# Performance work log

Hardware: AMD Instinct MI355X
Metric: run time of the kernel (lower is better)

## Reference

```python
import jax, jax.numpy as jnp
import numpy as np

B, N, NT, MAXN, M2, TF = 1, 4096, 2, 100, 16, 4
NA = N // NT          # atoms per type
J = NT * MAXN         # total neighbor slots per atom
GDIM = 100
D = M2 * GDIM         # fitting-net input dim
FH = 240


def _mlp_emb(x, w0, b0, w1, b1, w2, b2):
    h = jnp.tanh(x @ w0 + b0)
    h = jnp.tanh(h @ w1 + b1)
    return jnp.tanh(h @ w2 + b2)


def _mlp_fit(x, w0, b0, w1, b1, w2, b2):
    h = jnp.tanh(x @ w0 + b0)
    h = jnp.tanh(h @ w1 + b1)
    return h @ w2 + b2


def setup_inputs() -> dict:
    key = jax.random.key(0)
    ks = jax.random.split(key, 16)

    def w(k, shape):
        return (jax.random.normal(k, shape, jnp.float32) / np.float32(np.sqrt(shape[-2])))

    return {
        "Ri": jax.random.normal(ks[0], (B, N, J, 4), jnp.float32),
        "dfeat": jax.random.normal(ks[1], (B, N, J, 4, 3), jnp.float32),
        "ImageDR": jax.random.normal(ks[2], (B, N, J, 3), jnp.float32),
        "type_vector": jax.random.uniform(ks[3], (NT, TF), jnp.float32),
        "ew0": w(ks[4], (1 + TF, 25)), "eb0": jnp.zeros((25,), jnp.float32),
        "ew1": w(ks[5], (25, 50)), "eb1": jnp.zeros((50,), jnp.float32),
        "ew2": w(ks[6], (50, GDIM)), "eb2": jnp.zeros((GDIM,), jnp.float32),
        "fw0": w(ks[7], (NT, D, FH)), "fb0": jnp.zeros((NT, FH), jnp.float32),
        "fw1": w(ks[8], (NT, FH, FH)), "fb1": jnp.zeros((NT, FH), jnp.float32),
        "fw2": w(ks[9], (NT, FH, 1)),
        "fb2": jnp.full((NT, 1), -3.0, jnp.float32),  # energy_shift folded into bias
        "list_neigh": jax.random.randint(ks[10], (B, N, J), 0, N + 1, dtype=jnp.int32),
    }


def reference(Ri, dfeat, ImageDR, type_vector, ew0, eb0, ew1, eb1, ew2, eb2,
              fw0, fb0, fw1, fb1, fw2, fb2, list_neigh):
    # type embedding feature, repeated per neighbor slot: [J, TF]
    temb = jnp.repeat(type_vector, MAXN, axis=0)

    def energy(Ri_):
        parts = []
        for t in range(NT):  # small fixed loop over atom types
            a = Ri_[:, t * NA:(t + 1) * NA]                      # [B,NA,J,4]
            x = jnp.concatenate(
                [a[..., :1], jnp.broadcast_to(temb, (B, NA, J, TF))], axis=-1)
            G = _mlp_emb(x, ew0, eb0, ew1, eb1, ew2, eb2)        # [B,NA,J,GDIM]
            xa = jnp.einsum('bnjc,bnjg->bncg', a, G) / (MAXN * NT)
            dr = jnp.einsum('bncg,bncm->bngm', xa, xa[..., :M2]).reshape(B, NA, D)
            parts.append(_mlp_fit(dr, fw0[t], fb0[t], fw1[t], fb1[t], fw2[t], fb2[t]))
        return jnp.concatenate(parts, axis=1)                    # [B,N,1]

    Ei = energy(Ri)
    Etot = jnp.sum(Ei, axis=1)                                   # [B,1]

    # dE/dRi (autograd.grad with ones mask == grad of sum(Ei))
    dE = jax.grad(lambda r: energy(r).sum())(Ri)                 # [B,N,J,4]
    dE_dx = jnp.einsum('bnjc,bnjcd->bnjd', dE, dfeat)            # [B,N,J,3]
    F = -jnp.sum(dE_dx, axis=2)                                  # -dE @ Ri_d (all slots)

    mask = (list_neigh > 0).astype(Ri.dtype)[..., None]
    contrib = dE_dx * mask                                       # only real neighbors
    idx = jnp.clip(list_neigh - 1, 0, N - 1)

    def scat(Fb, ib, cb):
        return Fb.at[ib.reshape(-1)].add(cb.reshape(-1, 3))
    F = jax.vmap(scat)(F, idx, contrib)

    dr0, dr1, dr2 = ImageDR[..., 0], ImageDR[..., 1], ImageDR[..., 2]
    c0, c1, c2 = contrib[..., 0], contrib[..., 1], contrib[..., 2]
    s = lambda v: jnp.sum(v, axis=(1, 2))
    V00, V11, V22 = s(dr0 * c0), s(dr1 * c1), s(dr2 * c2)
    V01, V02, V12 = s(dr0 * c1), s(dr0 * c2), s(dr1 * c2)
    Virial = jnp.stack([V00, V01, V02, V01, V11, V12, V02, V12, V22], axis=-1)

    return (Etot, jnp.squeeze(Ei, 2), F, Virial)
```

## Files before the change

### kernel.cpp

```cpp
#include <hip/hip_runtime.h>

#define NATOMS 4096
#define NTYPES 2
#define NA 2048
#define MAXNB 100
#define JN 200
#define TFD 4
#define E0 25
#define E1 50
#define GD 100
#define M2D 16
#define DD 1600
#define FHD 240
#define INV200 (1.0f/200.0f)

#define OUT_EI 1
#define OUT_F 4097
#define OUT_V 16385

#define WS_Q 0L
#define WS_FW1T 0L
#define WS_DRB 6553600L
#define WS_XA 9830400L
#define WS_P 11468800L
#define WS_FH0 13107200L
#define WS_FH1 14090240L
#define WS_DH0GB 15073280L
#define WS_FH0B 15597568L
#define WS_FW0TB 16121856L
#define WS_FW0B 16531456L
#define WS_FW1TB 16941056L

#define NK 1024
#define S_MIN (-8.0f)
#define S_H 0.015625f
#define S_INVH 64.0f
#define HCH 104
__device__ float4 g_tab4[NTYPES * NK * GD];
__device__ float2 g_th1[NTYPES * NK * E1];
__device__ _Float16 h_tab[NTYPES * NK * HCH * 4];

typedef __attribute__((ext_vector_type(8))) short bf16x8;
typedef __attribute__((ext_vector_type(4))) float f32x4;
typedef __attribute__((ext_vector_type(2))) _Float16 h16x2;

#if defined(__has_builtin)
#if __has_builtin(__builtin_amdgcn_fdot2)
#define HAVE_FDOT2 1
#endif
#endif
#ifdef HAVE_FDOT2
#define FDOT2(a, b, c) __builtin_amdgcn_fdot2((a), (b), (c), false)
#else
__device__ __forceinline__ float fdot2_sw(h16x2 a, h16x2 b, float c) {
    return fmaf((float)a[0], (float)b[0], fmaf((float)a[1], (float)b[1], c));
}
#define FDOT2(a, b, c) fdot2_sw((a), (b), (c))
#endif

__device__ __forceinline__ h16x2 as_h2(unsigned u) {
    union { unsigned u; h16x2 h; } v; v.u = u; return v.h;
}

__device__ __forceinline__ unsigned h2u(h16x2 h) {
    union { h16x2 h; unsigned u; } v; v.h = h; return v.u;
}

__device__ __forceinline__ float ftanh(float x) {
    float ax = fabsf(x);
    float e = __expf(-2.0f * ax);
    float t = (1.0f - e) / (1.0f + e);
    return copysignf(t, x);
}

__device__ __forceinline__ unsigned short f2b(float f) {
    union { float f; unsigned u; } v; v.f = f;
    unsigned r = (v.u + 0x7FFF + ((v.u >> 16) & 1)) >> 16;
    return (unsigned short)r;
}

__device__ __forceinline__ float4 ntload4(const float4* p) {
    f32x4 v = __builtin_nontemporal_load((const f32x4*)p);
    float4 r; r.x = v.x; r.y = v.y; r.z = v.z; r.w = v.w;
    return r;
}

__global__ void k_setup(const float* __restrict__ fw0, const float* __restrict__ fw1,
                        unsigned short* __restrict__ fw0Tb, unsigned short* __restrict__ fw0b,
                        float* __restrict__ fw1T, unsigned short* __restrict__ fw1Tb) {
    int idx = blockIdx.x * 256 + threadIdx.x;
    if (idx < NTYPES * FHD * DD) {
        int t = idx / (FHD * DD);
        int r = idx % (FHD * DD);
        int o = r / DD, d = r % DD;
        fw0Tb[(long)t * 256 * DD + (long)o * DD + d] =
            f2b(fw0[(long)t * DD * FHD + (long)d * FHD + o]);
    }
    if (idx < NTYPES * DD * 256) {
        int t = idx / (DD * 256);
        int r = idx % (DD * 256);
        int d = r / 256, kk = r % 256;
        float v = (kk < FHD) ? fw0[(long)t * DD * FHD + (long)d * FHD + kk] : 0.f;
        fw0b[idx] = f2b(v);
    }
    if (idx < NTYPES * FHD * FHD) {
        int t = idx / (FHD * FHD);
        int r = idx % (FHD * FHD);
        int o = r / FHD, i = r % FHD;
        fw1T[idx] = fw1[(long)t * FHD * FHD + (long)i * FHD + o];
    }
    if (idx < NTYPES * FHD * 256) {
        int t = idx / (FHD * 256);
        int r = idx % (FHD * 256);
        int o = r / 256, kk = r % 256;
        float v = (kk < FHD) ? fw1[(long)t * FHD * FHD + (long)kk * FHD + o] : 0.f;
        fw1Tb[(long)t * 256 * 256 + (long)o * 256 + kk] = f2b(v);
    }
}

__global__ __launch_bounds__(256) void k_table_h(
    const float* __restrict__ ew0, const float* __restrict__ eb0,
    const float* __restrict__ ew1, const float* __restrict__ eb1,
    const float* __restrict__ tv)
{
    int idx = blockIdx.x * 256 + threadIdx.x;
    if (idx >= NTYPES * NK) return;
    int t = idx / NK, i = idx % NK;
    float s = S_MIN + (float)i * S_H;

    float h0[E0], t0[E0];
#pragma unroll
    for (int k = 0; k < E0; ++k) {
        float c = eb0[k];
#pragma unroll
        for (int f = 0; f < TFD; ++f) c = fmaf(tv[t * TFD + f], ew0[(1 + f) * E0 + k], c);
        float h = ftanh(fmaf(s, ew0[k], c));
        h0[k] = h;
        t0[k] = (1.f - h * h) * ew0[k];
    }
#pragma unroll 2
    for (int l = 0; l < E1; ++l) {
        float acc = eb1[l], dacc = 0.f;
#pragma unroll
        for (int k = 0; k < E0; ++k) {
            float w = ew1[k * E1 + l];
            acc = fmaf(h0[k], w, acc);
            dacc = fmaf(t0[k], w, dacc);
        }
        float h = ftanh(acc);
        g_th1[(long)idx * E1 + l] = make_float2(h, (1.f - h * h) * dacc);
    }
}

__global__ __launch_bounds__(256) void k_table_g(
    const float* __restrict__ ew2, const float* __restrict__ eb2)
{
    long idx = (long)blockIdx.x * 256 + threadIdx.x;
    if (idx >= (long)NTYPES * NK * GD) return;
    int g = idx % GD;
    long ti = idx / GD;
    int i = ti % NK;

    const float2* hv = g_th1 + ti * E1;
    float acc = eb2[g], dacc = 0.f;
#pragma unroll 5
    for (int l = 0; l < E1; ++l) {
        float2 x = hv[l];
        float w = ew2[l * GD + g];
        acc = fmaf(x.x, w, acc);
        dacc = fmaf(x.y, w, dacc);
    }
    float G = ftanh(acc);
    float dv = (1.f - G * G) * dacc;

    float2* f2 = (float2*)g_tab4;
    long e = ti * GD + g;
    f2[2 * e] = make_float2(G, dv);
    if (i > 0) f2[2 * (e - GD) + 1] = make_float2(G, dv);
}

__global__ __launch_bounds__(256) void k_table_h16() {
    long idx = (long)blockIdx.x * 256 + threadIdx.x;
    if (idx >= (long)NTYPES * NK * HCH) return;
    int g = idx % HCH;
    long ti = idx / HCH;
    _Float16* dst = h_tab + idx * 4;
    if (g >= GD) {
        dst[0] = (_Float16)0.f; dst[1] = (_Float16)0.f;
        dst[2] = (_Float16)0.f; dst[3] = (_Float16)0.f;
        return;
    }
    float4 r = g_tab4[ti * GD + g];
    dst[0] = (_Float16)r.x;
    dst[1] = (_Float16)(r.z - r.x);
    dst[2] = (_Float16)r.y;
    dst[3] = (_Float16)r.w;
}

__device__ __forceinline__ int hermite6(float s,
    float& c01, float& c10, float& c11,
    float& d00, float& d10, float& d11)
{
    float x = (s - S_MIN) * S_INVH;
    x = fminf(fmaxf(x, 0.f), (float)(NK - 1) - 1e-3f);
    int i = (int)x;
    float u = x - (float)i;
    float um = 1.f - u;
    c01 = u * u * (3.f - 2.f * u);
    c10 = S_H * u * um * um;
    c11 = S_H * u * u * (u - 1.f);
    d00 = (6.f * u * u - 6.f * u) * S_INVH;
    d10 = fmaf(3.f * u, u, fmaf(-4.f, u, 1.f));
    d11 = fmaf(3.f * u, u, -2.f * u);
    return i;
}

__global__ __launch_bounds__(256) void k1_emb(
    const float* __restrict__ Ri,
    unsigned short* __restrict__ drb, float* __restrict__ xa_ws)
{
    __shared__ float4 a4s[JN];
    __shared__ uint2 cpak[JN];
    __shared__ int rowoff[JN];
    __shared__ float xar[4 * 400];
    __shared__ float xas[400];

    int tid = threadIdx.x;
    int lane = tid & 63;
    int w = tid >> 6;
    int n = blockIdx.x;

    if (tid < JN) {
        float4 a = ((const float4*)Ri)[(long)n * JN + tid];
        a4s[tid] = a;
        float c01, c10, c11, d00, d10, d11;
        int ik = hermite6(a.x, c01, c10, c11, d00, d10, d11);
        rowoff[tid] = ((tid / MAXNB) * NK + ik) * (HCH / 2);
        h16x2 cP; cP[0] = (_Float16)1.f;  cP[1] = (_Float16)c01;
        h16x2 cQ; cQ[0] = (_Float16)c10;  cQ[1] = (_Float16)c11;
        cpak[tid] = make_uint2(h2u(cP), h2u(cQ));
    }
    __syncthreads();

    float xe0 = 0.f, xe1 = 0.f, xe2 = 0.f, xe3 = 0.f;
    float xo0 = 0.f, xo1 = 0.f, xo2 = 0.f, xo3 = 0.f;

#pragma unroll 4
    for (int ii = 0; ii < 50; ++ii) {
        int j = w * 50 + ii;
        uint2 cc = cpak[j];
        const uint4* row4 = (const uint4*)h_tab + rowoff[j];
        if (lane < 50) {
            uint4 v = row4[lane];
            float4 a = a4s[j];
            float Ge = FDOT2(as_h2(v.y), as_h2(cc.y), FDOT2(as_h2(v.x), as_h2(cc.x), 0.f));
            float Go = FDOT2(as_h2(v.w), as_h2(cc.y), FDOT2(as_h2(v.z), as_h2(cc.x), 0.f));
            xe0 = fmaf(a.x, Ge, xe0); xe1 = fmaf(a.y, Ge, xe1);
            xe2 = fmaf(a.z, Ge, xe2); xe3 = fmaf(a.w, Ge, xe3);
            xo0 = fmaf(a.x, Go, xo0); xo1 = fmaf(a.y, Go, xo1);
            xo2 = fmaf(a.z, Go, xo2); xo3 = fmaf(a.w, Go, xo3);
        }
    }

    float* xw = xar + w * 400;
    if (lane < 50) {
        *(float2*)&xw[0 * GD + 2 * lane] = make_float2(xe0, xo0);
        *(float2*)&xw[1 * GD + 2 * lane] = make_float2(xe1, xo1);
        *(float2*)&xw[2 * GD + 2 * lane] = make_float2(xe2, xo2);
        *(float2*)&xw[3 * GD + 2 * lane] = make_float2(xe3, xo3);
    }
    __syncthreads();

    for (int i = tid; i < 400; i += 256) {
        float v = (xar[i] + xar[400 + i] + xar[800 + i] + xar[1200 + i]) * INV200;
        xas[i] = v;
        xa_ws[(long)n * 400 + i] = v;
    }
    __syncthreads();

    for (int i = tid; i < DD; i += 256) {
        int gg = i / M2D, m = i % M2D;
        float v = 0.f;
#pragma unroll
        for (int c = 0; c < 4; ++c) v = fmaf(xas[c * GD + gg], xas[c * GD + m], v);
        drb[(long)n * DD + i] = f2b(v);
    }
}

__global__ __launch_bounds__(256) void mgemm(
    const unsigned short* __restrict__ Ab, const unsigned short* __restrict__ BTb,
    const float* __restrict__ biasb, float* __restrict__ Cb, unsigned short* __restrict__ Cbf,
    int M, int N, int K, int Npad,
    long sA, long sBT, long sBias, long sC, long sCbf, int do_tanh)
{
    int t = blockIdx.z;
    const unsigned short* A = Ab + (long)t * sA;
    const unsigned short* BT = BTb + (long)t * sBT;
    const float* bias = biasb ? biasb + (long)t * sBias : nullptr;
    float* C = Cb + (long)t * sC;
    unsigned short* Cb16 = Cbf ? Cbf + (long)t * sCbf : nullptr;

    __shared__ __align__(16) unsigned short As[64 * 72];
    __shared__ __align__(16) unsigned short Bs[64 * 72];

    int tid = threadIdx.x;
    int m0 = blockIdx.x * 64;
    int n0 = blockIdx.y * 64;

    int lane = tid & 63;
    int w = tid >> 6;
    int wm = (w & 1) * 32;
    int wn = (w >> 1) * 32;
    int fm = lane & 15;
    int q = lane >> 4;

    f32x4 acc[2][2] = {};

    int sr = tid >> 2;
    int sc = tid & 3;

    const unsigned short* Ar = A + (long)(m0 + sr) * K + sc * 8;
    const unsigned short* Br = BT + (long)(n0 + sr) * K + sc * 8;
    unsigned short* Asw = As + sr * 72 + sc * 8;
    unsigned short* Bsw = Bs + sr * 72 + sc * 8;

    for (int k0 = 0; k0 < K; k0 += 64) {
        uint4 av0 = *(const uint4*)(Ar + k0);
        uint4 av1 = *(const uint4*)(Ar + k0 + 32);
        uint4 bv0 = *(const uint4*)(Br + k0);
        uint4 bv1 = *(const uint4*)(Br + k0 + 32);
        __syncthreads();
        *(uint4*)(Asw) = av0;
        *(uint4*)(Asw + 32) = av1;
        *(uint4*)(Bsw) = bv0;
        *(uint4*)(Bsw + 32) = bv1;
        __syncthreads();
#pragma unroll
        for (int kk = 0; kk < 64; kk += 32) {
            bf16x8 af0 = *(const bf16x8*)(As + (wm + fm) * 72 + kk + q * 8);
            bf16x8 af1 = *(const bf16x8*)(As + (wm + 16 + fm) * 72 + kk + q * 8);
            bf16x8 bg0 = *(const bf16x8*)(Bs + (wn + fm) * 72 + kk + q * 8);
            bf16x8 bg1 = *(const bf16x8*)(Bs + (wn + 16 + fm) * 72 + kk + q * 8);
            acc[0][0] = __builtin_amdgcn_mfma_f32_16x16x32_bf16(af0, bg0, acc[0][0], 0, 0, 0);
            acc[0][1] = __builtin_amdgcn_mfma_f32_16x16x32_bf16(af0, bg1, acc[0][1], 0, 0, 0);
            acc[1][0] = __builtin_amdgcn_mfma_f32_16x16x32_bf16(af1, bg0, acc[1][0], 0, 0, 0);
            acc[1][1] = __builtin_amdgcn_mfma_f32_16x16x32_bf16(af1, bg1, acc[1][1], 0, 0, 0);
        }
    }

#pragma unroll
    for (int i = 0; i < 2; ++i) {
#pragma unroll
        for (int j = 0; j < 2; ++j) {
            int col = n0 + wn + j * 16 + fm;
            int rb = m0 + wm + i * 16 + q * 4;
            bool ok = col < N;
            float bv = (bias && ok) ? bias[col] : 0.f;
#pragma unroll
            for (int r = 0; r < 4; ++r) {
                float v = acc[i][j][r] + bv;
                if (do_tanh) v = ftanh(v);
                if (ok) C[(long)(rb + r) * N + col] = v;
                if (Cb16) Cb16[(long)(rb + r) * Npad + col] = ok ? f2b(v) : (unsigned short)0;
            }
        }
    }
}

__global__ __launch_bounds__(256) void k3a(
    const float* __restrict__ fh0, const float* __restrict__ fh1,
    const float* __restrict__ fw1T, const float* __restrict__ fw2, const float* __restrict__ fb2,
    float* __restrict__ out, unsigned short* __restrict__ dh0gb)
{
    int n = blockIdx.x;
    int t = n / NA;
    int tid = threadIdx.x;
    __shared__ float u1s[FHD];
    __shared__ float red[256];

    float p = 0.f;
    if (tid < FHD) {
        float h1v = fh1[(long)n * FHD + tid];
        float w2v = fw2[t * FHD + tid];
        p = h1v * w2v;
        u1s[tid] = w2v * (1.f - h1v * h1v);
    }
    red[tid] = p;
    __syncthreads();
    for (int off = 128; off > 0; off >>= 1) {
        if (tid < off) red[tid] += red[tid + off];
        __syncthreads();
    }
    if (tid == 0) {
        float e = red[0] + fb2[t];
        out[OUT_EI + n] = e;
        atomicAdd(out, e);
    }
    float val = 0.f;
    if (tid < FHD) {
        const float* wT = fw1T + (long)t * FHD * FHD;
        float acc = 0.f;
        for (int o = 0; o < FHD; ++o) acc = fmaf(u1s[o], wT[o * FHD + tid], acc);
        float h0v = fh0[(long)n * FHD + tid];
        val = acc * (1.f - h0v * h0v);
    }
    dh0gb[(long)n * 256 + tid] = (tid < FHD) ? f2b(val) : (unsigned short)0;
}

__global__ __launch_bounds__(256) void k3b(
    const float* __restrict__ Q, const float* __restrict__ xa, float* __restrict__ P4)
{
    int n = blockIdx.x;
    int tid = threadIdx.x;
    __shared__ float qs[DD];
    __shared__ float xs[400];
    for (int i = tid; i < DD; i += 256) qs[i] = Q[(long)n * DD + i];
    for (int i = tid; i < 400; i += 256) xs[i] = xa[(long)n * 400 + i];
    __syncthreads();
    for (int i = tid; i < 400; i += 256) {
        int c = i / GD, g = i % GD;
        float acc = 0.f;
        for (int m = 0; m < M2D; ++m) acc = fmaf(qs[g * M2D + m], xs[c * GD + m], acc);
        if (g < M2D) {
            for (int g2 = 0; g2 < GD; ++g2) acc = fmaf(qs[g2 * M2D + g], xs[c * GD + g2], acc);
        }
        P4[((long)n * GD + g) * 4 + c] = acc * INV200;
    }
}

__device__ __forceinline__ void k4_tail(
    int n, int j, float4 a,
    float M10, float M11, float M12, float M13,
    float M20, float M21, float M22, float M23,
    const float* __restrict__ dfeat, const float* __restrict__ ImageDR,
    const int* __restrict__ list_neigh, float* __restrict__ out, int ql,
    float& f0, float& f1, float& f2v,
    float& v00, float& v01, float& v02, float& v11, float& v12, float& v22)
{
    float ds = a.x * M20 + a.y * M21 + a.z * M22 + a.w * M23;
    float dEda0 = M10 + ds, dEda1 = M11, dEda2 = M12, dEda3 = M13;

    long item = (long)n * JN + j;
    if (ql < 3) {
        const float* dfp = dfeat + item * 12 + ql;
        float w0 = __builtin_nontemporal_load(dfp);
        float w1 = __builtin_nontemporal_load(dfp + 3);
        float w2 = __builtin_nontemporal_load(dfp + 6);
        float w3 = __builtin_nontemporal_load(dfp + 9);
        float dEdx = dEda0 * w0 + dEda1 * w1 + dEda2 * w2 + dEda3 * w3;

        if (ql == 0) f0 += dEdx;
        else if (ql == 1) f1 += dEdx;
        else f2v += dEdx;

        int ln = __builtin_nontemporal_load(list_neigh + item);
        if (ln > 0) {
            int ii2 = ln - 1;
            if (ii2 > NATOMS - 1) ii2 = NATOMS - 1;
            atomicAdd(&out[OUT_F + ii2 * 3 + ql], dEdx);
            float im0 = __builtin_nontemporal_load(ImageDR + item * 3);
            float im1 = __builtin_nontemporal_load(ImageDR + item * 3 + 1);
            float im2 = __builtin_nontemporal_load(ImageDR + item * 3 + 2);
            if (ql == 0) {
                v00 += im0 * dEdx;
            } else if (ql == 1) {
                v01 += im0 * dEdx; v11 += im1 * dEdx;
            } else {
                v02 += im0 * dEdx; v12 += im1 * dEdx; v22 += im2 * dEdx;
            }
        }
    }
}

__global__ __launch_bounds__(256, 4) void k4(
    const float* __restrict__ Ri, const float* __restrict__ dfeat,
    const float* __restrict__ ImageDR, const int* __restrict__ list_neigh,
    const float4* __restrict__ P4ws, float* __restrict__ out)
{
    __shared__ float4 a4s[JN];
    __shared__ float4 P4s[HCH];
    __shared__ float fred[4][3];
    __shared__ float vred[4][6];
    __shared__ float vacc[6];

    int tid = threadIdx.x;
    int lane = tid & 63;
    int w = tid >> 6;
    int n = blockIdx.x;

    if (tid < JN) a4s[tid] = ntload4(&((const float4*)Ri)[(long)n * JN + tid]);
    if (tid < HCH)
        P4s[tid] = (tid < GD) ? ntload4(&P4ws[(long)n * GD + tid])
                              : make_float4(0.f, 0.f, 0.f, 0.f);
    __syncthreads();

    int ql = lane & 3;
    int qid = w * 16 + (lane >> 2);

    float f0 = 0.f, f1 = 0.f, f2v = 0.f;
    float v00 = 0.f, v01 = 0.f, v02 = 0.f, v11 = 0.f, v12 = 0.f, v22 = 0.f;

    for (int pass = 0; pass < 4; ++pass) {
        int j;
        if (pass < 3) {
            j = pass * 64 + qid;
        } else {
            if (qid & 7) break;
            j = 192 + (qid >> 3);
        }

        float4 a = a4s[j];
        float c01, c10, c11, d00, d10, d11;
        int ik = hermite6(a.x, c01, c10, c11, d00, d10, d11);
        const uint4* row4 = (const uint4*)h_tab + (long)((j / MAXNB) * NK + ik) * (HCH / 2);

        h16x2 cP; cP[0] = (_Float16)1.f;   cP[1] = (_Float16)c01;
        h16x2 cQ; cQ[0] = (_Float16)c10;   cQ[1] = (_Float16)c11;
        h16x2 cR; cR[0] = (_Float16)0.f;   cR[1] = (_Float16)(-d00);
        h16x2 cS; cS[0] = (_Float16)d10;   cS[1] = (_Float16)d11;

        float M10 = 0.f, M11 = 0.f, M12 = 0.f, M13 = 0.f;
        float M20 = 0.f, M21 = 0.f, M22 = 0.f, M23 = 0.f;

        uint4 r[13];
#pragma unroll
        for (int i2 = 0; i2 < 13; ++i2) r[i2] = row4[4 * i2 + ql];
        __builtin_amdgcn_sched_barrier(0);

#pragma unroll
        for (int i2 = 0; i2 < 13; ++i2) {
            int ca = 8 * i2 + 2 * ql;
            float4 pa = P4s[ca];
            float4 pb = P4s[ca + 1];
            float G1 = FDOT2(as_h2(r[i2].y), cQ, FDOT2(as_h2(r[i2].x), cP, 0.f));
            float D1 = FDOT2(as_h2(r[i2].y), cS, FDOT2(as_h2(r[i2].x), cR, 0.f));
            M10 = fmaf(pa.x, G1, M10); M11 = fmaf(pa.y, G1, M11);
            M12 = fmaf(pa.z, G1, M12); M13 = fmaf(pa.w, G1, M13);
            M20 = fmaf(pa.x, D1, M20); M21 = fmaf(pa.y, D1, M21);
            M22 = fmaf(pa.z, D1, M22); M23 = fmaf(pa.w, D1, M23);
            float G2 = FDOT2(as_h2(r[i2].w), cQ, FDOT2(as_h2(r[i2].z), cP, 0.f));
            float D2 = FDOT2(as_h2(r[i2].w), cS, FDOT2(as_h2(r[i2].z), cR, 0.f));
            M10 = fmaf(pb.x, G2, M10); M11 = fmaf(pb.y, G2, M11);
            M12 = fmaf(pb.z, G2, M12); M13 = fmaf(pb.w, G2, M13);
            M20 = fmaf(pb.x, D2, M20); M21 = fmaf(pb.y, D2, M21);
            M22 = fmaf(pb.z, D2, M22); M23 = fmaf(pb.w, D2, M23);
        }
        __builtin_amdgcn_sched_barrier(0);

#pragma unroll
        for (int mask = 1; mask <= 2; mask <<= 1) {
            M10 += __shfl_xor(M10, mask); M11 += __shfl_xor(M11, mask);
            M12 += __shfl_xor(M12, mask); M13 += __shfl_xor(M13, mask);
            M20 += __shfl_xor(M20, mask); M21 += __shfl_xor(M21, mask);
            M22 += __shfl_xor(M22, mask); M23 += __shfl_xor(M23, mask);
        }

        k4_tail(n, j, a, M10, M11, M12, M13, M20, M21, M22, M23,
                dfeat, ImageDR, list_neigh, out, ql, f0, f1, f2v,
                v00, v01, v02, v11, v12, v22);
    }

#pragma unroll
    for (int mask = 32; mask > 0; mask >>= 1) {
        f0 += __shfl_xor(f0, mask);
        f1 += __shfl_xor(f1, mask);
        f2v += __shfl_xor(f2v, mask);
        v00 += __shfl_xor(v00, mask);
        v01 += __shfl_xor(v01, mask);
        v02 += __shfl_xor(v02, mask);
        v11 += __shfl_xor(v11, mask);
        v12 += __shfl_xor(v12, mask);
        v22 += __shfl_xor(v22, mask);
    }
    if (lane == 0) {
        fred[w][0] = f0; fred[w][1] = f1; fred[w][2] = f2v;
        vred[w][0] = v00; vred[w][1] = v01; vred[w][2] = v02;
        vred[w][3] = v11; vred[w][4] = v12; vred[w][5] = v22;
    }
    __syncthreads();
    if (tid < 3) {
        float s = fred[0][tid] + fred[1][tid] + fred[2][tid] + fred[3][tid];
        atomicAdd(&out[OUT_F + n * 3 + tid], -s);
    }
    if (tid < 6) {
        vacc[tid] = vred[0][tid] + vred[1][tid] + vred[2][tid] + vred[3][tid];
    }
    __syncthreads();
    if (tid < 9) {
        const int vmap[9] = {0, 1, 2, 1, 3, 4, 2, 4, 5};
        atomicAdd(&out[OUT_V + tid], vacc[vmap[tid]]);
    }
}

extern "C" void kernel_launch(void* const* d_in, const int* in_sizes, int n_in,
                              void* d_out, int out_size, void* d_ws, size_t ws_size,
                              hipStream_t stream) {
    const float* Ri = (const float*)d_in[0];
    const float* dfeat = (const float*)d_in[1];
    const float* ImageDR = (const float*)d_in[2];
    const float* tv = (const float*)d_in[3];
    const float* ew0 = (const float*)d_in[4];
    const float* eb0 = (const float*)d_in[5];
    const float* ew1 = (const float*)d_in[6];
    const float* eb1 = (const float*)d_in[7];
    const float* ew2 = (const float*)d_in[8];
    const float* eb2 = (const float*)d_in[9];
    const float* fw0 = (const float*)d_in[10];
    const float* fb0 = (const float*)d_in[11];
    const float* fw1 = (const float*)d_in[12];
    const float* fb1 = (const float*)d_in[13];
    const float* fw2 = (const float*)d_in[14];
    const float* fb2 = (const float*)d_in[15];
    const int* list_neigh = (const int*)d_in[16];

    float* out = (float*)d_out;
    float* ws = (float*)d_ws;
    float* Q = ws + WS_Q;
    float* fw1T = ws + WS_FW1T;
    unsigned short* drb = (unsigned short*)(ws + WS_DRB);
    float* xa = ws + WS_XA;
    float* P = ws + WS_P;
    float* fh0 = ws + WS_FH0;
    float* fh1 = ws + WS_FH1;
    unsigned short* dh0gb = (unsigned short*)(ws + WS_DH0GB);
    unsigned short* fh0b = (unsigned short*)(ws + WS_FH0B);
    unsigned short* fw0Tb = (unsigned short*)(ws + WS_FW0TB);
    unsigned short* fw0b = (unsigned short*)(ws + WS_FW0B);
    unsigned short* fw1Tb = (unsigned short*)(ws + WS_FW1TB);

    hipMemsetAsync(d_out, 0, (size_t)out_size * sizeof(float), stream);

    k_setup<<<(NTYPES * DD * 256 + 255) / 256, 256, 0, stream>>>(
        fw0, fw1, fw0Tb, fw0b, fw1T, fw1Tb);
    k_table_h<<<(NTYPES * NK + 255) / 256, 256, 0, stream>>>(ew0, eb0, ew1, eb1, tv);
    k_table_g<<<(NTYPES * NK * GD + 255) / 256, 256, 0, stream>>>(ew2, eb2);
    k_table_h16<<<(NTYPES * NK * HCH + 255) / 256, 256, 0, stream>>>();

    k1_emb<<<NATOMS, 256, 0, stream>>>(Ri, drb, xa);

    mgemm<<<dim3(32, 4, 2), 256, 0, stream>>>(
        drb, fw0Tb, fb0, fh0, fh0b,
        2048, 240, 1600, 256,
        2048L * 1600, 256L * 1600, 240L, 2048L * 240, 2048L * 256, 1);
    mgemm<<<dim3(32, 4, 2), 256, 0, stream>>>(
        fh0b, fw1Tb, fb1, fh1, nullptr,
        2048, 240, 256, 0,
        2048L * 256, 256L * 256, 240L, 2048L * 240, 0L, 1);

    k3a<<<NATOMS, 256, 0, stream>>>(fh0, fh1, fw1T, fw2, fb2, out, dh0gb);

    mgemm<<<dim3(32, 25, 2), 256, 0, stream>>>(
        dh0gb, fw0b, nullptr, Q, nullptr,
        2048, 1600, 256, 0,
        2048L * 256, 1600L * 256, 0L, 2048L * 1600, 0L, 0);

    k3b<<<NATOMS, 256, 0, stream>>>(Q, xa, P);

    k4<<<NATOMS, 256, 0, stream>>>(Ri, dfeat, ImageDR, list_neigh,
        (const float4*)P, out);
}
```

Before: 437.3 us.

## Move fitting-net layer-1 backprop matvec into bf16 MFMA GEMM with tanh-derivative epilogue

The per-atom scalar matvec in k3a (u1 times fw1 transposed, then times 1-h0^2) is replaced by a batched bf16 MFMA GEMM. k3a now only writes u1 as padded bf16, and a new mgemm mode multiplies by (1-x^2) in the epilogue while writing the bf16 dh0 directly. k_setup builds a padded bf16 copy of fw1 instead of the fp32 transpose. k4 launch bounds are also raised to 6 blocks per SM, which may raise register pressure, and rounding u1 and fw1 to bf16 lowers precision.

```diff
diff --git a/kernel.cpp b/kernel.cpp
--- a/kernel.cpp
+++ b/kernel.cpp
@@ -19,8 +19,9 @@
 #define OUT_V 16385
 
 #define WS_Q 0L
-#define WS_FW1T 0L
+#define WS_FW1NB 0L
 #define WS_DRB 6553600L
+#define WS_U1B 6553600L
 #define WS_XA 9830400L
 #define WS_P 11468800L
 #define WS_FH0 13107200L
@@ -87,7 +88,7 @@
 
 __global__ void k_setup(const float* __restrict__ fw0, const float* __restrict__ fw1,
                         unsigned short* __restrict__ fw0Tb, unsigned short* __restrict__ fw0b,
-                        float* __restrict__ fw1T, unsigned short* __restrict__ fw1Tb) {
+                        unsigned short* __restrict__ fw1Tb, unsigned short* __restrict__ fw1Nb) {
     int idx = blockIdx.x * 256 + threadIdx.x;
     if (idx < NTYPES * FHD * DD) {
         int t = idx / (FHD * DD);
@@ -103,18 +104,19 @@
         float v = (kk < FHD) ? fw0[(long)t * DD * FHD + (long)d * FHD + kk] : 0.f;
         fw0b[idx] = f2b(v);
     }
-    if (idx < NTYPES * FHD * FHD) {
-        int t = idx / (FHD * FHD);
-        int r = idx % (FHD * FHD);
-        int o = r / FHD, i = r % FHD;
-        fw1T[idx] = fw1[(long)t * FHD * FHD + (long)i * FHD + o];
-    }
     if (idx < NTYPES * FHD * 256) {
         int t = idx / (FHD * 256);
         int r = idx % (FHD * 256);
         int o = r / 256, kk = r % 256;
         float v = (kk < FHD) ? fw1[(long)t * FHD * FHD + (long)kk * FHD + o] : 0.f;
         fw1Tb[(long)t * 256 * 256 + (long)o * 256 + kk] = f2b(v);
+    }
+    if (idx < NTYPES * 256 * 256) {
+        int t = idx / (256 * 256);
+        int r = idx % (256 * 256);
+        int i = r / 256, kk = r % 256;
+        float v = (i < FHD && kk < FHD) ? fw1[(long)t * FHD * FHD + (long)i * FHD + kk] : 0.f;
+        fw1Nb[(long)t * 256 * 256 + (long)i * 256 + kk] = f2b(v);
     }
 }
 
@@ -290,15 +292,17 @@
 __global__ __launch_bounds__(256) void mgemm(
     const unsigned short* __restrict__ Ab, const unsigned short* __restrict__ BTb,
     const float* __restrict__ biasb, float* __restrict__ Cb, unsigned short* __restrict__ Cbf,
+    const float* __restrict__ Xb,
     int M, int N, int K, int Npad,
-    long sA, long sBT, long sBias, long sC, long sCbf, int do_tanh)
+    long sA, long sBT, long sBias, long sC, long sCbf, long sX, int mode)
 {
     int t = blockIdx.z;
     const unsigned short* A = Ab + (long)t * sA;
     const unsigned short* BT = BTb + (long)t * sBT;
     const float* bias = biasb ? biasb + (long)t * sBias : nullptr;
-    float* C = Cb + (long)t * sC;
+    float* C = Cb ? Cb + (long)t * sC : nullptr;
     unsigned short* Cb16 = Cbf ? Cbf + (long)t * sCbf : nullptr;
+    const float* X = Xb ? Xb + (long)t * sX : nullptr;
 
     __shared__ __align__(16) unsigned short As[64 * 72];
     __shared__ __align__(16) unsigned short Bs[64 * 72];
@@ -359,8 +363,13 @@
 #pragma unroll
             for (int r = 0; r < 4; ++r) {
                 float v = acc[i][j][r] + bv;
-                if (do_tanh) v = ftanh(v);
-                if (ok) C[(long)(rb + r) * N + col] = v;
+                if (mode == 1) {
+                    v = ftanh(v);
+                } else if (mode == 2 && ok) {
+                    float x = X[(long)(rb + r) * N + col];
+                    v *= (1.f - x * x);
+                }
+                if (ok && C) C[(long)(rb + r) * N + col] = v;
                 if (Cb16) Cb16[(long)(rb + r) * Npad + col] = ok ? f2b(v) : (unsigned short)0;
             }
         }
@@ -368,23 +377,23 @@
 }
 
 __global__ __launch_bounds__(256) void k3a(
-    const float* __restrict__ fh0, const float* __restrict__ fh1,
-    const float* __restrict__ fw1T, const float* __restrict__ fw2, const float* __restrict__ fb2,
-    float* __restrict__ out, unsigned short* __restrict__ dh0gb)
+    const float* __restrict__ fh1, const float* __restrict__ fw2,
+    const float* __restrict__ fb2,
+    float* __restrict__ out, unsigned short* __restrict__ u1b)
 {
     int n = blockIdx.x;
     int t = n / NA;
     int tid = threadIdx.x;
-    __shared__ float u1s[FHD];
     __shared__ float red[256];
 
-    float p = 0.f;
+    float p = 0.f, u1 = 0.f;
     if (tid < FHD) {
         float h1v = fh1[(long)n * FHD + tid];
         float w2v = fw2[t * FHD + tid];
         p = h1v * w2v;
-        u1s[tid] = w2v * (1.f - h1v * h1v);
-    }
+        u1 = w2v * (1.f - h1v * h1v);
+    }
+    u1b[(long)n * 256 + tid] = (tid < FHD) ? f2b(u1) : (unsigned short)0;
     red[tid] = p;
     __syncthreads();
     for (int off = 128; off > 0; off >>= 1) {
@@ -396,15 +405,6 @@
         out[OUT_EI + n] = e;
         atomicAdd(out, e);
     }
-    float val = 0.f;
-    if (tid < FHD) {
-        const float* wT = fw1T + (long)t * FHD * FHD;
-        float acc = 0.f;
-        for (int o = 0; o < FHD; ++o) acc = fmaf(u1s[o], wT[o * FHD + tid], acc);
-        float h0v = fh0[(long)n * FHD + tid];
-        val = acc * (1.f - h0v * h0v);
-    }
-    dh0gb[(long)n * 256 + tid] = (tid < FHD) ? f2b(val) : (unsigned short)0;
 }
 
 __global__ __launch_bounds__(256) void k3b(
@@ -472,7 +472,7 @@
     }
 }
 
-__global__ __launch_bounds__(256, 4) void k4(
+__global__ __launch_bounds__(256, 6) void k4(
     const float* __restrict__ Ri, const float* __restrict__ dfeat,
     const float* __restrict__ ImageDR, const int* __restrict__ list_neigh,
     const float4* __restrict__ P4ws, float* __restrict__ out)
@@ -616,8 +616,9 @@
     float* out = (float*)d_out;
     float* ws = (float*)d_ws;
     float* Q = ws + WS_Q;
-    float* fw1T = ws + WS_FW1T;
+    unsigned short* fw1Nb = (unsigned short*)(ws + WS_FW1NB);
     unsigned short* drb = (unsigned short*)(ws + WS_DRB);
+    unsigned short* u1b = (unsigned short*)(ws + WS_U1B);
     float* xa = ws + WS_XA;
     float* P = ws + WS_P;
     float* fh0 = ws + WS_FH0;
@@ -631,7 +632,7 @@
     hipMemsetAsync(d_out, 0, (size_t)out_size * sizeof(float), stream);
 
     k_setup<<<(NTYPES * DD * 256 + 255) / 256, 256, 0, stream>>>(
-        fw0, fw1, fw0Tb, fw0b, fw1T, fw1Tb);
+        fw0, fw1, fw0Tb, fw0b, fw1Tb, fw1Nb);
     k_table_h<<<(NTYPES * NK + 255) / 256, 256, 0, stream>>>(ew0, eb0, ew1, eb1, tv);
     k_table_g<<<(NTYPES * NK * GD + 255) / 256, 256, 0, stream>>>(ew2, eb2);
     k_table_h16<<<(NTYPES * NK * HCH + 255) / 256, 256, 0, stream>>>();
@@ -639,20 +640,25 @@
     k1_emb<<<NATOMS, 256, 0, stream>>>(Ri, drb, xa);
 
     mgemm<<<dim3(32, 4, 2), 256, 0, stream>>>(
-        drb, fw0Tb, fb0, fh0, fh0b,
+        drb, fw0Tb, fb0, fh0, fh0b, nullptr,
         2048, 240, 1600, 256,
-        2048L * 1600, 256L * 1600, 240L, 2048L * 240, 2048L * 256, 1);
+        2048L * 1600, 256L * 1600, 240L, 2048L * 240, 2048L * 256, 0L, 1);
     mgemm<<<dim3(32, 4, 2), 256, 0, stream>>>(
-        fh0b, fw1Tb, fb1, fh1, nullptr,
+        fh0b, fw1Tb, fb1, fh1, nullptr, nullptr,
         2048, 240, 256, 0,
-        2048L * 256, 256L * 256, 240L, 2048L * 240, 0L, 1);
-
-    k3a<<<NATOMS, 256, 0, stream>>>(fh0, fh1, fw1T, fw2, fb2, out, dh0gb);
+        2048L * 256, 256L * 256, 240L, 2048L * 240, 0L, 0L, 1);
+
+    k3a<<<NATOMS, 256, 0, stream>>>(fh1, fw2, fb2, out, u1b);
+
+    mgemm<<<dim3(32, 4, 2), 256, 0, stream>>>(
+        u1b, fw1Nb, nullptr, nullptr, dh0gb, fh0,
+        2048, 240, 256, 256,
+        2048L * 256, 256L * 256, 0L, 0L, 2048L * 256, 2048L * 240, 2);
 
     mgemm<<<dim3(32, 25, 2), 256, 0, stream>>>(
-        dh0gb, fw0b, nullptr, Q, nullptr,
+        dh0gb, fw0b, nullptr, Q, nullptr, nullptr,
         2048, 1600, 256, 0,
-        2048L * 256, 1600L * 256, 0L, 2048L * 1600, 0L, 0);
+        2048L * 256, 1600L * 256, 0L, 2048L * 1600, 0L, 0L, 0);
 
     k3b<<<NATOMS, 256, 0, stream>>>(Q, xa, P);
 
```

Measured after the change: 675.8 us. 1.55x slower.
